# Optimization experiments

Hardware: AMD Instinct MI355X
Metric: run time of the kernel (lower is better)

Reference implementation:

```python
import jax, jax.numpy as jnp
import numpy as np
import math

H, D, DFF = 12, 768, 3072
DH = D // H  # 64
B, T = 4, 2048
EPS = 1e-5


def setup_inputs() -> dict:
    key = jax.random.key(0)
    ks = jax.random.split(key, 12)
    randw = lambda k, *d: jax.random.normal(k, d, jnp.float32) / math.sqrt(d[-1])
    return {
        "X": jax.random.normal(ks[0], (B, T, D), jnp.float32),
        "w_q": randw(ks[1], H, DH, D),
        "w_k": randw(ks[2], H, DH, D),
        "w_v": randw(ks[3], H, DH, D),
        "w_o": randw(ks[4], DH * H, D),
        "W1": jax.random.normal(ks[5], (DFF, D), jnp.float32) * 0.02,
        "b1": jnp.zeros((DFF,), jnp.float32),
        "W2": jax.random.normal(ks[6], (D, DFF), jnp.float32) * 0.02,
        "b2": jnp.zeros((D,), jnp.float32),
        "g1": jnp.ones((D,), jnp.float32),
        "be1": jnp.zeros((D,), jnp.float32),
        "g2": jnp.ones((D,), jnp.float32),
        "be2": jnp.zeros((D,), jnp.float32),
    }


def layernorm(x, g, b):
    mu = jnp.mean(x, axis=-1, keepdims=True)
    var = jnp.var(x, axis=-1, keepdims=True)
    return (x - mu) * jax.lax.rsqrt(var + EPS) * g + b


def attention(x, w_q, w_k, w_v, w_o):
    # x: [n,t,c]
    q = jnp.einsum('ntc,hdc->nhtd', x, w_q)
    k = jnp.einsum('ntc,hdc->nhtd', x, w_k)
    v = jnp.einsum('ntc,hdc->nhtd', x, w_v)
    a = jnp.einsum('nhtd,nhsd->nhts', q, k) / math.sqrt(q.shape[3])
    t, s = a.shape[2], a.shape[3]
    forbidden = jnp.arange(t)[:, None] < jnp.arange(s)[None, :]
    a = jnp.where(forbidden, -jnp.inf, a)
    a = jax.nn.softmax(a, axis=3)
    y = jnp.einsum('nhts,nhsd->nthd', a, v).reshape(x.shape[0], t, -1)
    return y @ w_o


def reference(X, w_q, w_k, w_v, w_o, W1, b1, W2, b2, g1, be1, g2, be2):
    X = X + attention(layernorm(X, g1, be1), w_q, w_k, w_v, w_o)
    h = jax.nn.relu(layernorm(X, g2, be2) @ W1.T + b1)
    return X + h @ W2.T + b2
```

## Files before the change

kernel.cpp:

```cpp
#include <hip/hip_runtime.h>
#include <stdint.h>

#define B_   4
#define T_   2048
#define D_   768
#define H_   12
#define DH_  64
#define DFF_ 3072
#define NTOK_ (B_*T_)
#define QKVN_ (3*D_)

typedef unsigned short u16;
typedef unsigned int u32;
typedef __bf16 bf16x8 __attribute__((ext_vector_type(8)));
typedef float  f32x4  __attribute__((ext_vector_type(4)));

__device__ __forceinline__ u16 f2bf(float f) {
  union { float f; unsigned u; } v; v.f = f;
  return (u16)((v.u + 0x7fffu + ((v.u >> 16) & 1u)) >> 16);
}

__device__ __forceinline__ float fast_exp2(float x) {
#if __has_builtin(__builtin_amdgcn_exp2f)
  return __builtin_amdgcn_exp2f(x);
#else
  return exp2f(x);
#endif
}

__device__ __forceinline__ float fast_rcp(float x) {
#if __has_builtin(__builtin_amdgcn_rcpf)
  return __builtin_amdgcn_rcpf(x);
#else
  return 1.0f / x;
#endif
}

__device__ __forceinline__ void gload_lds16(const void* g, void* l) {
  __builtin_amdgcn_global_load_lds(
      (__attribute__((address_space(1))) unsigned int*)(void*)g,
      (__attribute__((address_space(3))) unsigned int*)l, 16, 0, 0);
}

template<bool BIAS, bool RELU, bool RES, bool BF16OUT, bool QSCALE, int BN,
         bool VTRANS>
__global__ __launch_bounds__(256) void gemm_bt(
    const u16* __restrict__ A, const u16* __restrict__ Bw,
    const float* __restrict__ bias, const float* __restrict__ res,
    void* __restrict__ outp, u16* __restrict__ vtp, int M, int N, int K)
{
  constexpr int NI  = BN / 32;
  constexpr int NBG = BN / 64;
  __shared__ u16 lA[2 * 128 * 32];
  __shared__ u16 lB[2 * BN * 32];
  const int tid  = threadIdx.x;
  const int lane = tid & 63;
  const int wave = tid >> 6;
  const int quad = lane >> 4;
  const int l15  = lane & 15;
  const int mBase = blockIdx.x * 128;
  const int nBase = blockIdx.y * BN;
  const int wm = (wave >> 1) * 64;
  const int wn = (wave & 1) * (BN / 2);

  const f32x4 fz = {0.f, 0.f, 0.f, 0.f};
  f32x4 acc[4][NI];
#pragma unroll
  for (int i = 0; i < 4; i++)
#pragma unroll
    for (int j = 0; j < NI; j++) acc[i][j] = fz;

  const u16* gA[2];
  int cA[2];
#pragma unroll
  for (int i = 0; i < 2; i++) {
    cA[i] = tid + i * 256;
    const int row = cA[i] >> 2, j = (cA[i] & 3) ^ ((row >> 1) & 3);
    gA[i] = A + (size_t)(mBase + row) * K + j * 8;
  }
  const u16* gB[NBG];
  int cB[NBG];
#pragma unroll
  for (int g = 0; g < NBG; g++) {
    cB[g] = tid + g * 256;
    const int row = cB[g] >> 2, j = (cB[g] & 3) ^ ((row >> 1) & 3);
    gB[g] = Bw + (size_t)(nBase + row) * K + j * 8;
  }

  const int ca = (quad ^ ((l15 >> 1) & 3)) * 8;

  for (int kt = 0; kt < K; kt += 64) {
#pragma unroll
    for (int i = 0; i < 2; i++) {
      gload_lds16(gA[i] + kt,      lA + cA[i] * 8);
      gload_lds16(gA[i] + kt + 32, lA + 128 * 32 + cA[i] * 8);
    }
#pragma unroll
    for (int g = 0; g < NBG; g++) {
      gload_lds16(gB[g] + kt,      lB + cB[g] * 8);
      gload_lds16(gB[g] + kt + 32, lB + BN * 32 + cB[g] * 8);
    }
    __syncthreads();
#pragma unroll
    for (int hf = 0; hf < 2; hf++) {
      const u16* lAh = lA + hf * (128 * 32);
      const u16* lBh = lB + hf * (BN * 32);
      bf16x8 af[4], bfr[NI];
#pragma unroll
      for (int mi = 0; mi < 4; mi++)
        af[mi] = *(const bf16x8*)(lAh + (wm + mi * 16 + l15) * 32 + ca);
#pragma unroll
      for (int ni = 0; ni < NI; ni++)
        bfr[ni] = *(const bf16x8*)(lBh + (wn + ni * 16 + l15) * 32 + ca);
#pragma unroll
      for (int mi = 0; mi < 4; mi++)
#pragma unroll
        for (int ni = 0; ni < NI; ni++)
          acc[mi][ni] = __builtin_amdgcn_mfma_f32_16x16x32_bf16(
              af[mi], bfr[ni], acc[mi][ni], 0, 0, 0);
    }
    __syncthreads();
  }

#pragma unroll
  for (int mi = 0; mi < 4; mi++) {
#pragma unroll
    for (int ni = 0; ni < NI; ni++) {
      const int col = nBase + wn + ni * 16 + l15;
      if (VTRANS && col >= 2 * D_) {
        const int n  = col - 2 * D_;
        const int hh = n >> 6, dd = n & 63;
        const int row0 = mBase + wm + mi * 16 + quad * 4;
        const int bb = row0 >> 11, tt = row0 & (T_ - 1);
        const int tperm = (tt & ~31) + 8 * quad + 4 * (mi & 1);
        ushort4 pk;
        pk.x = f2bf(acc[mi][ni][0]); pk.y = f2bf(acc[mi][ni][1]);
        pk.z = f2bf(acc[mi][ni][2]); pk.w = f2bf(acc[mi][ni][3]);
        *(ushort4*)(vtp + ((size_t)((bb * H_ + hh) * DH_ + dd)) * T_ + tperm) = pk;
        continue;
      }
      float bv = 0.f;
      if (BIAS) bv = bias[col];
#pragma unroll
      for (int r = 0; r < 4; r++) {
        const int row = mBase + wm + mi * 16 + quad * 4 + r;
        float v = acc[mi][ni][r];
        if (BIAS) v += bv;
        if (RELU) v = fmaxf(v, 0.f);
        if (RES)  v += res[(size_t)row * N + col];
        if (QSCALE && col < D_) v *= 0.180336880f;
        if (BF16OUT) ((u16*)outp)[(size_t)row * N + col] = f2bf(v);
        else        ((float*)outp)[(size_t)row * N + col] = v;
      }
    }
  }
}

__device__ __forceinline__ void attn_round(
    const u16* __restrict__ lKc, const u16* __restrict__ lVc,
    int s0, int qw0, int quad, int l15,
    int kc0, int kc1,
    const bf16x8& q0, const bf16x8& q1,
    f32x4 (&o)[4], float& ls)
{
  const f32x4 fz = {0.f, 0.f, 0.f, 0.f};
  f32x4 s[4];
#pragma unroll
  for (int ni = 0; ni < 4; ni++) {
    const int rb = (ni * 16 + l15) * 64;
    const bf16x8 k0 = *(const bf16x8*)(lKc + rb + kc0);
    const bf16x8 k1 = *(const bf16x8*)(lKc + rb + kc1);
    f32x4 t = fz;
    t = __builtin_amdgcn_mfma_f32_16x16x32_bf16(k0, q0, t, 0, 0, 0);
    t = __builtin_amdgcn_mfma_f32_16x16x32_bf16(k1, q1, t, 0, 0, 0);
    s[ni] = t;
  }

  const bool nm = (s0 + 63 > qw0);
  union { __bf16 h[16]; bf16x8 v[2]; } P;
  float ls0 = 0.f, ls1 = 0.f;
  if (nm) {
    const int qidx = qw0 + l15;
#pragma unroll
    for (int ni = 0; ni < 4; ni++) {
      const int sbase = s0 + ni * 16 + quad * 4;
#pragma unroll
      for (int r = 0; r < 4; r++) {
        float v = fast_exp2(s[ni][r]);
        if (sbase + r > qidx) v = 0.f;
        P.h[ni * 4 + r] = (__bf16)v;
        if (r & 1) ls1 += v; else ls0 += v;
      }
    }
  } else {
#pragma unroll
    for (int ni = 0; ni < 4; ni++) {
#pragma unroll
      for (int r = 0; r < 4; r++) {
        float v = fast_exp2(s[ni][r]);
        P.h[ni * 4 + r] = (__bf16)v;
        if (r & 1) ls1 += v; else ls0 += v;
      }
    }
  }
  ls += ls0 + ls1;

#pragma unroll
  for (int dt = 0; dt < 4; dt++) {
    const int rb = (dt * 16 + l15) * 64;
    const bf16x8 v0 = *(const bf16x8*)(lVc + rb + kc0);
    const bf16x8 v1 = *(const bf16x8*)(lVc + rb + kc1);
    o[dt] = __builtin_amdgcn_mfma_f32_16x16x32_bf16(v0, P.v[0], o[dt], 0, 0, 0);
    o[dt] = __builtin_amdgcn_mfma_f32_16x16x32_bf16(v1, P.v[1], o[dt], 0, 0, 0);
  }
}

__global__ __launch_bounds__(256) void attn_kernel(
    const u16* __restrict__ qkv, const u16* __restrict__ vt, u16* __restrict__ Y)
{
  __shared__ u16 lK[2][64 * 64];
  __shared__ u16 lV[2][64 * 64];
  const int tid  = threadIdx.x;
  const int lane = tid & 63;
  const int wave = tid >> 6;
  const int quad = lane >> 4;
  const int l15  = lane & 15;
  const int lid = (int)(blockIdx.x + 16 * blockIdx.y + 192 * blockIdx.z);
  const int nid = (lid & 7) * 96 + (lid >> 3);
  const int pi = nid & 15;
  const int h  = (nid >> 4) % 12;
  const int b  = nid / 192;
  const int tH = 31 - pi, tL = pi;
  const int njsH = tH + 1;
  const int total = njsH + tL + 1;
  const int qwH = tH * 64 + wave * 16;
  const int qwL = tL * 64 + wave * 16;

  const int sw  = l15 & 7;
  const int kc0 = (quad ^ sw) * 8;
  const int kc1 = ((4 + quad) ^ sw) * 8;

  bf16x8 qH0, qH1, qL0, qL1;
  {
    const u16* qp = qkv + (size_t)(b * T_ + qwH + l15) * QKVN_ + h * DH_ + quad * 8;
    qH0 = *(const bf16x8*)(qp);
    qH1 = *(const bf16x8*)(qp + 32);
    const u16* qp2 = qkv + (size_t)(b * T_ + qwL + l15) * QKVN_ + h * DH_ + quad * 8;
    qL0 = *(const bf16x8*)(qp2);
    qL1 = *(const bf16x8*)(qp2 + 32);
  }

  const f32x4 fz = {0.f, 0.f, 0.f, 0.f};
  f32x4 oH[4], oL[4];
#pragma unroll
  for (int i = 0; i < 4; i++) { oH[i] = fz; oL[i] = fz; }
  float lsH = 0.f, lsL = 0.f;

  const int c0 = tid, c1 = tid + 256;
  const int r0 = c0 >> 3, j0 = (c0 & 7) ^ (r0 & 7);
  const int r1 = c1 >> 3, j1 = (c1 & 7) ^ (r1 & 7);
  const u16* gK0 = qkv + (size_t)(b * T_ + r0) * QKVN_ + D_ + h * DH_ + j0 * 8;
  const u16* gK1 = qkv + (size_t)(b * T_ + r1) * QKVN_ + D_ + h * DH_ + j1 * 8;
  const u16* gV0 = vt + (size_t)((b * H_ + h) * DH_ + r0) * T_ + j0 * 8;
  const u16* gV1 = vt + (size_t)((b * H_ + h) * DH_ + r1) * T_ + j1 * 8;

  gload_lds16(gK0, lK[0] + c0 * 8);
  gload_lds16(gK1, lK[0] + c1 * 8);
  gload_lds16(gV0, lV[0] + c0 * 8);
  gload_lds16(gV1, lV[0] + c1 * 8);

  for (int i = 0; i < total; i++) {
    const int cur = i & 1;
    __syncthreads();

    if (i + 1 < total) {
      const int sn = (i + 1 < njsH) ? (i + 1) : (i + 1 - njsH);
      const size_t s1 = (size_t)sn * 64;
      const int nb = cur ^ 1;
      gload_lds16(gK0 + s1 * QKVN_, lK[nb] + c0 * 8);
      gload_lds16(gK1 + s1 * QKVN_, lK[nb] + c1 * 8);
      gload_lds16(gV0 + s1,         lV[nb] + c0 * 8);
      gload_lds16(gV1 + s1,         lV[nb] + c1 * 8);
    }

    const u16* lKc = lK[cur];
    const u16* lVc = lV[cur];
    if (i < njsH) {
      attn_round(lKc, lVc, i * 64, qwH, quad, l15, kc0, kc1,
                 qH0, qH1, oH, lsH);
    } else {
      attn_round(lKc, lVc, (i - njsH) * 64, qwL, quad, l15, kc0, kc1,
                 qL0, qL1, oL, lsL);
    }
  }

  lsH += __shfl_xor(lsH, 16); lsH += __shfl_xor(lsH, 32);
  lsL += __shfl_xor(lsL, 16); lsL += __shfl_xor(lsL, 32);
  const float rlH = fast_rcp(lsH);
  const float rlL = fast_rcp(lsL);

#pragma unroll
  for (int dt = 0; dt < 4; dt++) {
    const int dbase = h * DH_ + dt * 16 + quad * 4;
    ushort4 pa, pb;
    pa.x = f2bf(oH[dt][0] * rlH); pa.y = f2bf(oH[dt][1] * rlH);
    pa.z = f2bf(oH[dt][2] * rlH); pa.w = f2bf(oH[dt][3] * rlH);
    pb.x = f2bf(oL[dt][0] * rlL); pb.y = f2bf(oL[dt][1] * rlL);
    pb.z = f2bf(oL[dt][2] * rlL); pb.w = f2bf(oL[dt][3] * rlL);
    *(ushort4*)(Y + (size_t)(b * T_ + qwH + l15) * D_ + dbase) = pa;
    *(ushort4*)(Y + (size_t)(b * T_ + qwL + l15) * D_ + dbase) = pb;
  }
}

__device__ __forceinline__ void ln_row(
    const float* __restrict__ X, const float* __restrict__ g,
    const float* __restrict__ be, u16* __restrict__ out, int row)
{
  const float* x = X + (size_t)row * D_;
  const int t = threadIdx.x;
  const float v0 = x[t], v1 = x[t + 256], v2 = x[t + 512];
  float s = v0 + v1 + v2;
  float sq = v0 * v0 + v1 * v1 + v2 * v2;
#pragma unroll
  for (int off = 1; off < 64; off <<= 1) {
    s  += __shfl_xor(s, off);
    sq += __shfl_xor(sq, off);
  }
  __shared__ float ws_[4], wq_[4];
  const int wv = t >> 6, lane = t & 63;
  if (lane == 0) { ws_[wv] = s; wq_[wv] = sq; }
  __syncthreads();
  s  = ws_[0] + ws_[1] + ws_[2] + ws_[3];
  sq = wq_[0] + wq_[1] + wq_[2] + wq_[3];
  const float mean = s * (1.f / 768.f);
  const float var  = sq * (1.f / 768.f) - mean * mean;
  const float rstd = rsqrtf(var + 1e-5f);
  u16* o = out + (size_t)row * D_;
  int c = t;
  o[c] = f2bf((v0 - mean) * rstd * g[c] + be[c]); c += 256;
  o[c] = f2bf((v1 - mean) * rstd * g[c] + be[c]); c += 256;
  o[c] = f2bf((v2 - mean) * rstd * g[c] + be[c]);
}

__global__ __launch_bounds__(256) void ln_kernel(
    const float* __restrict__ X, const float* __restrict__ g,
    const float* __restrict__ be, u16* __restrict__ out)
{
  ln_row(X, g, be, out, blockIdx.x);
}

__global__ __launch_bounds__(256) void prep_kernel(
    const float* __restrict__ X, const float* __restrict__ g1,
    const float* __restrict__ be1, u16* __restrict__ xln,
    const float* __restrict__ w_q, const float* __restrict__ w_k,
    const float* __restrict__ w_v, const float* __restrict__ W1,
    const float* __restrict__ W2, const float* __restrict__ w_o,
    u16* __restrict__ wqkv, u16* __restrict__ W1b,
    u16* __restrict__ W2b, u16* __restrict__ woT)
{
  if (blockIdx.x < NTOK_) {
    ln_row(X, g1, be1, xln, blockIdx.x);
    return;
  }
  const int id = blockIdx.x - NTOK_;
  if (id < 144) {
    __shared__ float tile[64][65];
    const int bx = id % 12, by = id / 12;
    const int rr0 = by * 64, cc0 = bx * 64;
    for (int idx = threadIdx.x; idx < 4096; idx += 256) {
      const int i = idx >> 6, j = idx & 63;
      tile[i][j] = w_o[(size_t)(rr0 + i) * D_ + cc0 + j];
    }
    __syncthreads();
    for (int idx = threadIdx.x; idx < 4096; idx += 256) {
      const int i = idx >> 6, j = idx & 63;
      woT[(size_t)(cc0 + i) * D_ + rr0 + j] = f2bf(tile[j][i]);
    }
  } else {
    const int WQN = H_ * DH_ * D_;
    const int i = (id - 144) * 256 + threadIdx.x;
    if (i < 3 * WQN) {
      const float* src = (i < WQN) ? w_q : (i < 2 * WQN ? w_k : w_v);
      const int off = (i < WQN) ? i : (i < 2 * WQN ? i - WQN : i - 2 * WQN);
      wqkv[i] = f2bf(src[off]);
    } else if (i < 3 * WQN + DFF_ * D_) {
      const int off = i - 3 * WQN;
      W1b[off] = f2bf(W1[off]);
    } else {
      const int off = i - 3 * WQN - DFF_ * D_;
      W2b[off] = f2bf(W2[off]);
    }
  }
}

extern "C" void kernel_launch(void* const* d_in, const int* in_sizes, int n_in,
                              void* d_out, int out_size, void* d_ws, size_t ws_size,
                              hipStream_t stream) {
  const float* X   = (const float*)d_in[0];
  const float* w_q = (const float*)d_in[1];
  const float* w_k = (const float*)d_in[2];
  const float* w_v = (const float*)d_in[3];
  const float* w_o = (const float*)d_in[4];
  const float* W1  = (const float*)d_in[5];
  const float* b1  = (const float*)d_in[6];
  const float* W2  = (const float*)d_in[7];
  const float* b2  = (const float*)d_in[8];
  const float* g1  = (const float*)d_in[9];
  const float* be1 = (const float*)d_in[10];
  const float* g2  = (const float*)d_in[11];
  const float* be2 = (const float*)d_in[12];
  float* out = (float*)d_out;

  char* ws = (char*)d_ws;
  u16*   qkv  = (u16*)(ws + 0);
  u16*   vt   = (u16*)(ws + 37748736);
  u16*   hbuf = (u16*)(ws + 0);
  u16*   xln  = (u16*)(ws + 50331648);
  u16*   Ybuf = (u16*)(ws + 62914560);
  float* X1   = (float*)(ws + 75497472);
  u16*   wqkv = (u16*)(ws + 100663296);
  u16*   woT  = (u16*)(ws + 104202240);
  u16*   W1b  = (u16*)(ws + 105381888);
  u16*   W2b  = (u16*)(ws + 110100480);

  prep_kernel<<<NTOK_ + 25488, 256, 0, stream>>>(
      X, g1, be1, xln, w_q, w_k, w_v, W1, W2, w_o, wqkv, W1b, W2b, woT);

  gemm_bt<false, false, false, true, true, 128, true>
      <<<dim3(64, 18), 256, 0, stream>>>(
      xln, wqkv, nullptr, nullptr, qkv, vt, NTOK_, QKVN_, D_);

  attn_kernel<<<dim3(16, 12, 4), 256, 0, stream>>>(qkv, vt, Ybuf);

  gemm_bt<false, false, true, false, false, 64, false>
      <<<dim3(64, 12), 256, 0, stream>>>(
      Ybuf, woT, nullptr, X, X1, nullptr, NTOK_, D_, D_);

  ln_kernel<<<NTOK_, 256, 0, stream>>>(X1, g2, be2, xln);

  gemm_bt<true, true, false, true, false, 256, false>
      <<<dim3(64, 12), 256, 0, stream>>>(
      xln, W1b, b1, nullptr, hbuf, nullptr, NTOK_, DFF_, D_);

  gemm_bt<true, false, true, false, false, 64, false>
      <<<dim3(64, 12), 256, 0, stream>>>(
      hbuf, W2b, b2, X1, out, nullptr, NTOK_, D_, DFF_);
}
```

Before: 373.0 us.

## Double-buffer LDS staging in narrow GEMMs and shrink FFN1 tile width

Adds a VPIPE template option that double-buffers the LDS tiles for the BN=64 GEMMs (output projection and FFN2). Global-to-LDS loads for tile t+2 are issued while tile t is computed, with explicit vmcnt waits and barriers, so load latency overlaps the MFMA work. The FFN1 GEMM also drops from BN=256 to BN=128, doubling its grid. The cost is more shared memory per block and a hand-coded vmcnt count that only holds for BN=64, which a static_assert enforces.

```diff
diff --git a/kernel.cpp b/kernel.cpp
--- a/kernel.cpp
+++ b/kernel.cpp
@@ -43,16 +43,17 @@
 }
 
 template<bool BIAS, bool RELU, bool RES, bool BF16OUT, bool QSCALE, int BN,
-         bool VTRANS>
+         bool VTRANS, bool VPIPE>
 __global__ __launch_bounds__(256) void gemm_bt(
     const u16* __restrict__ A, const u16* __restrict__ Bw,
     const float* __restrict__ bias, const float* __restrict__ res,
     void* __restrict__ outp, u16* __restrict__ vtp, int M, int N, int K)
 {
-  constexpr int NI  = BN / 32;
-  constexpr int NBG = BN / 64;
-  __shared__ u16 lA[2 * 128 * 32];
-  __shared__ u16 lB[2 * BN * 32];
+  constexpr int NI   = BN / 32;
+  constexpr int NBG  = BN / 64;
+  constexpr int NBUF = VPIPE ? 2 : 1;
+  __shared__ u16 lA[NBUF][2 * 128 * 32];
+  __shared__ u16 lB[NBUF][2 * BN * 32];
   const int tid  = threadIdx.x;
   const int lane = tid & 63;
   const int wave = tid >> 6;
@@ -89,22 +90,24 @@
 
   const int ca = (quad ^ ((l15 >> 1) & 3)) * 8;
 
-  for (int kt = 0; kt < K; kt += 64) {
+  auto stage = [&](int kt, int buf) {
 #pragma unroll
     for (int i = 0; i < 2; i++) {
-      gload_lds16(gA[i] + kt,      lA + cA[i] * 8);
-      gload_lds16(gA[i] + kt + 32, lA + 128 * 32 + cA[i] * 8);
+      gload_lds16(gA[i] + kt,      lA[buf] + cA[i] * 8);
+      gload_lds16(gA[i] + kt + 32, lA[buf] + 128 * 32 + cA[i] * 8);
     }
 #pragma unroll
     for (int g = 0; g < NBG; g++) {
-      gload_lds16(gB[g] + kt,      lB + cB[g] * 8);
-      gload_lds16(gB[g] + kt + 32, lB + BN * 32 + cB[g] * 8);
-    }
-    __syncthreads();
+      gload_lds16(gB[g] + kt,      lB[buf] + cB[g] * 8);
+      gload_lds16(gB[g] + kt + 32, lB[buf] + BN * 32 + cB[g] * 8);
+    }
+  };
+
+  auto compute = [&](int buf) {
 #pragma unroll
     for (int hf = 0; hf < 2; hf++) {
-      const u16* lAh = lA + hf * (128 * 32);
-      const u16* lBh = lB + hf * (BN * 32);
+      const u16* lAh = lA[buf] + hf * (128 * 32);
+      const u16* lBh = lB[buf] + hf * (BN * 32);
       bf16x8 af[4], bfr[NI];
 #pragma unroll
       for (int mi = 0; mi < 4; mi++)
@@ -119,7 +122,28 @@
           acc[mi][ni] = __builtin_amdgcn_mfma_f32_16x16x32_bf16(
               af[mi], bfr[ni], acc[mi][ni], 0, 0, 0);
     }
-    __syncthreads();
+  };
+
+  if constexpr (VPIPE) {
+    static_assert(BN == 64, "VPIPE vmcnt count assumes 6 loads/stage");
+    const int nk = K >> 6;
+    stage(0, 0);
+    stage(64, 1);
+    for (int t = 0; t < nk; t++) {
+      if (t + 1 < nk) asm volatile("s_waitcnt vmcnt(6)" ::: "memory");
+      else            asm volatile("s_waitcnt vmcnt(0)" ::: "memory");
+      __builtin_amdgcn_s_barrier();
+      compute(t & 1);
+      __builtin_amdgcn_s_barrier();
+      if (t + 2 < nk) stage((t + 2) * 64, t & 1);
+    }
+  } else {
+    for (int kt = 0; kt < K; kt += 64) {
+      stage(kt, 0);
+      __syncthreads();
+      compute(0);
+      __syncthreads();
+    }
   }
 
 #pragma unroll
@@ -426,23 +450,23 @@
   prep_kernel<<<NTOK_ + 25488, 256, 0, stream>>>(
       X, g1, be1, xln, w_q, w_k, w_v, W1, W2, w_o, wqkv, W1b, W2b, woT);
 
-  gemm_bt<false, false, false, true, true, 128, true>
+  gemm_bt<false, false, false, true, true, 128, true, false>
       <<<dim3(64, 18), 256, 0, stream>>>(
       xln, wqkv, nullptr, nullptr, qkv, vt, NTOK_, QKVN_, D_);
 
   attn_kernel<<<dim3(16, 12, 4), 256, 0, stream>>>(qkv, vt, Ybuf);
 
-  gemm_bt<false, false, true, false, false, 64, false>
+  gemm_bt<false, false, true, false, false, 64, false, true>
       <<<dim3(64, 12), 256, 0, stream>>>(
       Ybuf, woT, nullptr, X, X1, nullptr, NTOK_, D_, D_);
 
   ln_kernel<<<NTOK_, 256, 0, stream>>>(X1, g2, be2, xln);
 
-  gemm_bt<true, true, false, true, false, 256, false>
-      <<<dim3(64, 12), 256, 0, stream>>>(
+  gemm_bt<true, true, false, true, false, 128, false, false>
+      <<<dim3(64, 24), 256, 0, stream>>>(
       xln, W1b, b1, nullptr, hbuf, nullptr, NTOK_, DFF_, D_);
 
-  gemm_bt<true, false, true, false, false, 64, false>
+  gemm_bt<true, false, true, false, false, 64, false, true>
       <<<dim3(64, 12), 256, 0, stream>>>(
       hbuf, W2b, b2, X1, out, nullptr, NTOK_, D_, DFF_);
 }
```

Result: faster. 337.4 us (-9.5%).
